# Kernel optimization log

Hardware: AMD Instinct MI355X
Metric: run time of the kernel (lower is better)

## Reference

```python
import jax, jax.numpy as jnp
import numpy as np

C = 512
NUM_HEADS = 8
HEAD_DIM = C // NUM_HEADS  # 64
BN_EPS = 1e-5


def setup_inputs() -> dict:
    key = jax.random.key(0)
    ks = jax.random.split(key, 12)
    B, H, W = 8, 32, 32
    s = 0.02
    return {
        "x": jax.random.normal(ks[0], (B, C, H, W), dtype=jnp.float32),
        "gamma": jnp.ones((C,), jnp.float32),
        "beta": jnp.zeros((C,), jnp.float32),
        "rmean": jnp.zeros((C,), jnp.float32),
        "rvar": jnp.ones((C,), jnp.float32),
        "wq": jax.random.normal(ks[1], (C, C), jnp.float32) * s,
        "bq": jnp.zeros((C,), jnp.float32),
        "wk": jax.random.normal(ks[2], (C, C), jnp.float32) * s,
        "bk": jnp.zeros((C,), jnp.float32),
        "wv": jax.random.normal(ks[3], (C, C), jnp.float32) * s,
        "bv": jnp.zeros((C,), jnp.float32),
        "wp": jax.random.normal(ks[4], (C, C), jnp.float32) * s,
        "bp": jnp.zeros((C,), jnp.float32),
    }


def _conv1x1(w, b, h):
    # 1x1 conv == per-pixel dense: (O,C) x (B,C,H,W) -> (B,O,H,W)
    return jnp.einsum('oc,bchw->bohw', w, h) + b[None, :, None, None]


def reference(x, gamma, beta, rmean, rvar, wq, bq, wk, bk, wv, bv, wp, bp):
    B, Cc, H, W = x.shape
    N = H * W
    # BatchNorm2d (eval mode, running stats)
    inv = gamma / jnp.sqrt(rvar + BN_EPS)
    h = x * inv[None, :, None, None] + (beta - rmean * inv)[None, :, None, None]
    q = _conv1x1(wq, bq, h).reshape(B, NUM_HEADS, HEAD_DIM, N)
    k = _conv1x1(wk, bk, h).reshape(B, NUM_HEADS, HEAD_DIM, N)
    v = _conv1x1(wv, bv, h).reshape(B, NUM_HEADS, HEAD_DIM, N)
    scale = 1.0 / np.sqrt(HEAD_DIM).astype(np.float32)
    attn = jnp.einsum('bhdn,bhdm->bhnm', q, k) * scale  # [B,heads,N,N]
    attn = jnp.clip(attn, -50.0, 50.0)
    attn = jax.nn.softmax(attn, axis=-1)
    out = jnp.einsum('bhnm,bhdm->bhdn', attn, v).reshape(B, Cc, H, W)
    out = _conv1x1(wp, bp, out)
    return x + out
```

## Files before the change

kernel.cpp:

```cpp
#include <hip/hip_runtime.h>
#include <stdint.h>

#define C_DIM 512
#define NHEADS 8
#define HDIM 64
#define BATCH 8
#define NPIX 1024
#define Q_PRESCALE 0.18033688011112042f

typedef __bf16 bf16x8 __attribute__((ext_vector_type(8)));
typedef float f32x4 __attribute__((ext_vector_type(4)));
typedef float f32x16 __attribute__((ext_vector_type(16)));

__device__ __forceinline__ unsigned short f2bf(float f) {
  union { float f; unsigned u; } v; v.f = f;
  unsigned r = v.u + 0x7fffu + ((v.u >> 16) & 1u);
  return (unsigned short)(r >> 16);
}

__device__ __forceinline__ void gl_lds16(const void* g, void* l) {
  __builtin_amdgcn_global_load_lds(
      (__attribute__((address_space(1))) void*)g,
      (__attribute__((address_space(3))) void*)l,
      16, 0, 0);
}

__global__ __launch_bounds__(256) void k_prep(const float* __restrict__ wq,
                                              const float* __restrict__ wk,
                                              const float* __restrict__ wv,
                                              const float* __restrict__ wp,
                                              unsigned short* __restrict__ wbf) {
  const int n = C_DIM * C_DIM;
  for (int i = blockIdx.x * blockDim.x + threadIdx.x; i < 4 * n;
       i += gridDim.x * blockDim.x) {
    const float* src = (i < n) ? wq : (i < 2 * n) ? wk : (i < 3 * n) ? wv : wp;
    wbf[i] = f2bf(src[i & (n - 1)]);
  }
}

__global__ __launch_bounds__(256) void k_bnT(const float* __restrict__ x,
                                             const float* __restrict__ gamma,
                                             const float* __restrict__ beta,
                                             const float* __restrict__ rmean,
                                             const float* __restrict__ rvar,
                                             unsigned short* __restrict__ hbT) {
  __shared__ unsigned short tile[64][72];
  const int b = blockIdx.z, c0 = blockIdx.y * 64, n0 = blockIdx.x * 64;
  const int t = threadIdx.x;
#pragma unroll
  for (int it = 0; it < 4; ++it) {
    int c = it * 16 + (t >> 4);
    int n = (t & 15) * 4;
    const float4 v = *(const float4*)&x[((size_t)b * C_DIM + c0 + c) * NPIX + n0 + n];
    int cc = c0 + c;
    float inv = gamma[cc] * rsqrtf(rvar[cc] + 1e-5f);
    float add = beta[cc] - rmean[cc] * inv;
    tile[c][n + 0] = f2bf(v.x * inv + add);
    tile[c][n + 1] = f2bf(v.y * inv + add);
    tile[c][n + 2] = f2bf(v.z * inv + add);
    tile[c][n + 3] = f2bf(v.w * inv + add);
  }
  __syncthreads();
#pragma unroll
  for (int it = 0; it < 2; ++it) {
    int n = it * 32 + (t >> 3);
    int cj = (t & 7) * 8;
    unsigned short tmp[8];
#pragma unroll
    for (int u = 0; u < 8; ++u) tmp[u] = tile[cj + u][n];
    uint4 pk;
    pk.x = (unsigned)tmp[0] | ((unsigned)tmp[1] << 16);
    pk.y = (unsigned)tmp[2] | ((unsigned)tmp[3] << 16);
    pk.z = (unsigned)tmp[4] | ((unsigned)tmp[5] << 16);
    pk.w = (unsigned)tmp[6] | ((unsigned)tmp[7] << 16);
    *(uint4*)&hbT[((size_t)b * NPIX + n0 + n) * C_DIM + c0 + cj] = pk;
  }
}

__global__ __launch_bounds__(256) void k_qkv(const unsigned short* __restrict__ wbf,
                                             const float* __restrict__ bq,
                                             const float* __restrict__ bk,
                                             const float* __restrict__ bv,
                                             const unsigned short* __restrict__ hbT,
                                             unsigned short* __restrict__ QT,
                                             unsigned short* __restrict__ KT,
                                             unsigned short* __restrict__ Vb) {
  __shared__ unsigned short Atile[128 * 32];
  __shared__ unsigned short Btile[128 * 32];
  const int which = blockIdx.z >> 3;
  const int b = blockIdx.z & 7;
  const int m0 = blockIdx.y * 128, n0 = blockIdx.x * 128;
  const unsigned short* W = wbf + (size_t)which * C_DIM * C_DIM;
  const int t = threadIdx.x, wave = t >> 6, lane = t & 63;
  const int wr = wave >> 1, wc = wave & 1;
  f32x4 acc[4][4] = {};

  const int st_row = lane >> 2;
  const int st_col = (((lane & 3) ^ ((lane >> 3) & 3))) * 8;

  for (int k0 = 0; k0 < C_DIM; k0 += 32) {
    __syncthreads();
#pragma unroll
    for (int it = 0; it < 2; ++it) {
      int q = wave + 4 * it;
      int row = q * 16 + st_row;
      gl_lds16(&W[(size_t)(m0 + row) * C_DIM + k0 + st_col], &Atile[q * 512]);
      gl_lds16(&hbT[((size_t)b * NPIX + n0 + row) * C_DIM + k0 + st_col], &Btile[q * 512]);
    }
    __syncthreads();
    bf16x8 af[4], bfr[4];
#pragma unroll
    for (int i = 0; i < 4; ++i) {
      int row = wr * 64 + i * 16 + (lane & 15);
      af[i] = *(const bf16x8*)&Atile[row * 32 + (((lane >> 4) ^ ((row >> 1) & 3)) * 8)];
    }
#pragma unroll
    for (int j = 0; j < 4; ++j) {
      int row = wc * 64 + j * 16 + (lane & 15);
      bfr[j] = *(const bf16x8*)&Btile[row * 32 + (((lane >> 4) ^ ((row >> 1) & 3)) * 8)];
    }
#pragma unroll
    for (int i = 0; i < 4; ++i)
#pragma unroll
      for (int j = 0; j < 4; ++j)
        acc[i][j] = __builtin_amdgcn_mfma_f32_16x16x32_bf16(af[i], bfr[j], acc[i][j], 0, 0, 0);
  }

  const float* bias = (which == 0) ? bq : (which == 1) ? bk : bv;
  if (which < 2) {
    unsigned short* T = (which == 0) ? QT : KT;
    const float qs = (which == 0) ? Q_PRESCALE : 1.0f;
#pragma unroll
    for (int i = 0; i < 4; ++i) {
      int o = m0 + wr * 64 + i * 16 + (lane >> 4) * 4;
      float b0 = bias[o + 0], b1 = bias[o + 1], b2 = bias[o + 2], b3 = bias[o + 3];
#pragma unroll
      for (int j = 0; j < 4; ++j) {
        int n = n0 + wc * 64 + j * 16 + (lane & 15);
        ushort4 pk;
        pk.x = f2bf((acc[i][j][0] + b0) * qs);
        pk.y = f2bf((acc[i][j][1] + b1) * qs);
        pk.z = f2bf((acc[i][j][2] + b2) * qs);
        pk.w = f2bf((acc[i][j][3] + b3) * qs);
        *(ushort4*)&T[((size_t)b * NPIX + n) * C_DIM + o] = pk;
      }
    }
  } else {
#pragma unroll
    for (int i = 0; i < 4; ++i) {
      int o = m0 + wr * 64 + i * 16 + (lane >> 4) * 4;
#pragma unroll
      for (int j = 0; j < 4; ++j) {
        int n = n0 + wc * 64 + j * 16 + (lane & 15);
#pragma unroll
        for (int r = 0; r < 4; ++r)
          Vb[((size_t)b * C_DIM + o + r) * NPIX + n] = f2bf(acc[i][j][r] + bias[o + r]);
      }
    }
  }
}

__global__ __launch_bounds__(256) void k_attn(const unsigned short* __restrict__ QT,
                                              const unsigned short* __restrict__ KT,
                                              const unsigned short* __restrict__ Vb,
                                              unsigned short* __restrict__ AOT) {
  const int bid = blockIdx.x;
  const int b = bid & 7, h = (bid >> 3) & 7, qt = bid >> 6;
  const int n0 = qt * 128;
  const int lane = threadIdx.x & 63, wave = threadIdx.x >> 6;
  const int l31 = lane & 31, hi = lane >> 5;

  bf16x8 qf[4];
  {
    const unsigned short* qbase =
        QT + ((size_t)b * NPIX + n0 + wave * 32 + l31) * C_DIM + h * HDIM + hi * 8;
#pragma unroll
    for (int kk = 0; kk < 4; ++kk) qf[kk] = *(const bf16x8*)(qbase + kk * 16);
  }

  union { unsigned u[4]; bf16x8 v; } ones;
  ones.u[0] = 0x3F803F80u; ones.u[1] = 0x3F803F80u;
  ones.u[2] = 0x3F803F80u; ones.u[3] = 0x3F803F80u;

  const unsigned short* kbase =
      KT + ((size_t)b * NPIX + l31) * C_DIM + h * HDIM + hi * 8;
  const unsigned short* vbase =
      Vb + ((size_t)b * C_DIM + h * HDIM) * NPIX + hi * 8;

  f32x16 oacc[2] = {};
  f32x16 rsacc = {};

  for (int m0 = 0; m0 < NPIX; m0 += 32) {
    f32x16 s = {};
#pragma unroll
    for (int kk = 0; kk < 4; ++kk) {
      bf16x8 kf = *(const bf16x8*)(kbase + (size_t)m0 * C_DIM + kk * 16);
      s = __builtin_amdgcn_mfma_f32_32x32x16_bf16(kf, qf[kk], s, 0, 0, 0);
    }
    unsigned w[8];
#pragma unroll
    for (int r2 = 0; r2 < 8; ++r2) {
      float e0 = exp2f(s[2 * r2]);
      float e1 = exp2f(s[2 * r2 + 1]);
      asm("v_cvt_pk_bf16_f32 %0, %1, %2" : "=v"(w[r2]) : "v"(e0), "v"(e1));
    }
    asm volatile("v_permlane32_swap_b32 %0, %1" : "+v"(w[0]), "+v"(w[2]));
    asm volatile("v_permlane32_swap_b32 %0, %1" : "+v"(w[1]), "+v"(w[3]));
    asm volatile("v_permlane32_swap_b32 %0, %1" : "+v"(w[4]), "+v"(w[6]));
    asm volatile("v_permlane32_swap_b32 %0, %1" : "+v"(w[5]), "+v"(w[7]));
    union U8 { unsigned u[4]; bf16x8 v; };
    U8 pa0, pa1;
    pa0.u[0] = w[0]; pa0.u[1] = w[1]; pa0.u[2] = w[2]; pa0.u[3] = w[3];
    pa1.u[0] = w[4]; pa1.u[1] = w[5]; pa1.u[2] = w[6]; pa1.u[3] = w[7];
    rsacc = __builtin_amdgcn_mfma_f32_32x32x16_bf16(pa0.v, ones.v, rsacc, 0, 0, 0);
    rsacc = __builtin_amdgcn_mfma_f32_32x32x16_bf16(pa1.v, ones.v, rsacc, 0, 0, 0);
#pragma unroll
    for (int dt = 0; dt < 2; ++dt) {
      const unsigned short* vrow = vbase + (size_t)(dt * 32 + l31) * NPIX + m0;
      bf16x8 v0 = *(const bf16x8*)(vrow);
      bf16x8 v1 = *(const bf16x8*)(vrow + 16);
      oacc[dt] = __builtin_amdgcn_mfma_f32_32x32x16_bf16(pa0.v, v0, oacc[dt], 0, 0, 0);
      oacc[dt] = __builtin_amdgcn_mfma_f32_32x32x16_bf16(pa1.v, v1, oacc[dt], 0, 0, 0);
    }
  }

  float inv[16];
#pragma unroll
  for (int r = 0; r < 16; ++r) inv[r] = 1.0f / rsacc[r];

  __bf16* obase = (__bf16*)(AOT + ((size_t)b * NPIX + n0 + wave * 32) * C_DIM +
                            h * HDIM + l31);
#pragma unroll
  for (int dt = 0; dt < 2; ++dt)
#pragma unroll
    for (int r = 0; r < 16; ++r) {
      int q = (r & 3) + 8 * (r >> 2) + 4 * hi;
      obase[(size_t)q * C_DIM + dt * 32] = (__bf16)(oacc[dt][r] * inv[r]);
    }
}

__global__ __launch_bounds__(256) void k_proj(const unsigned short* __restrict__ Wp,
                                              const float* __restrict__ bp,
                                              const unsigned short* __restrict__ AOT,
                                              const float* __restrict__ x,
                                              float* __restrict__ out) {
  __shared__ unsigned short Atile[128 * 32];
  __shared__ unsigned short Btile[128 * 32];
  const int b = blockIdx.z;
  const int m0 = blockIdx.y * 128, n0 = blockIdx.x * 128;
  const int t = threadIdx.x, wave = t >> 6, lane = t & 63;
  const int wr = wave >> 1, wc = wave & 1;
  f32x4 acc[4][4] = {};
  const int st_row = lane >> 2;
  const int st_col = (((lane & 3) ^ ((lane >> 3) & 3))) * 8;

  for (int k0 = 0; k0 < C_DIM; k0 += 32) {
    __syncthreads();
#pragma unroll
    for (int it = 0; it < 2; ++it) {
      int q = wave + 4 * it;
      int row = q * 16 + st_row;
      gl_lds16(&Wp[(size_t)(m0 + row) * C_DIM + k0 + st_col], &Atile[q * 512]);
      gl_lds16(&AOT[((size_t)b * NPIX + n0 + row) * C_DIM + k0 + st_col], &Btile[q * 512]);
    }
    __syncthreads();
    bf16x8 af[4], bfr[4];
#pragma unroll
    for (int i = 0; i < 4; ++i) {
      int row = wr * 64 + i * 16 + (lane & 15);
      af[i] = *(const bf16x8*)&Atile[row * 32 + (((lane >> 4) ^ ((row >> 1) & 3)) * 8)];
    }
#pragma unroll
    for (int j = 0; j < 4; ++j) {
      int row = wc * 64 + j * 16 + (lane & 15);
      bfr[j] = *(const bf16x8*)&Btile[row * 32 + (((lane >> 4) ^ ((row >> 1) & 3)) * 8)];
    }
#pragma unroll
    for (int i = 0; i < 4; ++i)
#pragma unroll
      for (int j = 0; j < 4; ++j)
        acc[i][j] = __builtin_amdgcn_mfma_f32_16x16x32_bf16(af[i], bfr[j], acc[i][j], 0, 0, 0);
  }

#pragma unroll
  for (int i = 0; i < 4; ++i) {
    int o = m0 + wr * 64 + i * 16 + (lane >> 4) * 4;
    float b0 = bp[o + 0], b1 = bp[o + 1], b2 = bp[o + 2], b3 = bp[o + 3];
#pragma unroll
    for (int j = 0; j < 4; ++j) {
      int n = n0 + wc * 64 + j * 16 + (lane & 15);
      size_t base = ((size_t)b * C_DIM + o) * NPIX + n;
      out[base + 0 * NPIX] = acc[i][j][0] + b0 + x[base + 0 * NPIX];
      out[base + 1 * NPIX] = acc[i][j][1] + b1 + x[base + 1 * NPIX];
      out[base + 2 * NPIX] = acc[i][j][2] + b2 + x[base + 2 * NPIX];
      out[base + 3 * NPIX] = acc[i][j][3] + b3 + x[base + 3 * NPIX];
    }
  }
}

extern "C" void kernel_launch(void* const* d_in, const int* in_sizes, int n_in,
                              void* d_out, int out_size, void* d_ws, size_t ws_size,
                              hipStream_t stream) {
  (void)in_sizes; (void)n_in; (void)out_size; (void)ws_size;
  const float* x     = (const float*)d_in[0];
  const float* gamma = (const float*)d_in[1];
  const float* beta  = (const float*)d_in[2];
  const float* rmean = (const float*)d_in[3];
  const float* rvar  = (const float*)d_in[4];
  const float* wq    = (const float*)d_in[5];
  const float* bq    = (const float*)d_in[6];
  const float* wk    = (const float*)d_in[7];
  const float* bk    = (const float*)d_in[8];
  const float* wv    = (const float*)d_in[9];
  const float* bv    = (const float*)d_in[10];
  const float* wp    = (const float*)d_in[11];
  const float* bp    = (const float*)d_in[12];

  unsigned short* ws  = (unsigned short*)d_ws;
  const size_t WSZ    = (size_t)C_DIM * C_DIM;
  const size_t BIG    = (size_t)BATCH * NPIX * C_DIM;
  unsigned short* wbf = ws;
  unsigned short* hbT = wbf + 4 * WSZ;
  unsigned short* QT  = hbT + BIG;
  unsigned short* KT  = QT + BIG;
  unsigned short* Vb  = KT + BIG;
  unsigned short* AOT = Vb + BIG;

  k_prep<<<dim3(512), dim3(256), 0, stream>>>(wq, wk, wv, wp, wbf);
  k_bnT<<<dim3(16, 8, 8), dim3(256), 0, stream>>>(x, gamma, beta, rmean, rvar, hbT);
  k_qkv<<<dim3(8, 4, 24), dim3(256), 0, stream>>>(wbf, bq, bk, bv, hbT, QT, KT, Vb);
  k_attn<<<dim3(512), dim3(256), 0, stream>>>(QT, KT, Vb, AOT);
  k_proj<<<dim3(8, 4, 8), dim3(256), 0, stream>>>(wbf + 3 * WSZ, bp, AOT, x, (float*)d_out);
}
```

Before: 196.6 us.

## Split attention over key halves with LDS double-buffered K/V and combine pass

```diff
diff --git a/kernel.cpp b/kernel.cpp
--- a/kernel.cpp
+++ b/kernel.cpp
@@ -163,10 +163,16 @@
 __global__ __launch_bounds__(256) void k_attn(const unsigned short* __restrict__ QT,
                                               const unsigned short* __restrict__ KT,
                                               const unsigned short* __restrict__ Vb,
-                                              unsigned short* __restrict__ AOT) {
+                                              unsigned short* __restrict__ OA,
+                                              unsigned short* __restrict__ OB,
+                                              float* __restrict__ rs) {
+  __shared__ unsigned short Ks[2][64 * 64];
+  __shared__ unsigned short Vs[2][64 * 64];
+
   const int bid = blockIdx.x;
-  const int b = bid & 7, h = (bid >> 3) & 7, qt = bid >> 6;
+  const int b = bid & 7, h = (bid >> 3) & 7, qt = (bid >> 6) & 7, ks = bid >> 9;
   const int n0 = qt * 128;
+  const int kbase0 = ks * 512;
   const int lane = threadIdx.x & 63, wave = threadIdx.x >> 6;
   const int l31 = lane & 31, hi = lane >> 5;
 
@@ -182,53 +188,76 @@
   ones.u[0] = 0x3F803F80u; ones.u[1] = 0x3F803F80u;
   ones.u[2] = 0x3F803F80u; ones.u[3] = 0x3F803F80u;
 
-  const unsigned short* kbase =
-      KT + ((size_t)b * NPIX + l31) * C_DIM + h * HDIM + hi * 8;
-  const unsigned short* vbase =
-      Vb + ((size_t)b * C_DIM + h * HDIM) * NPIX + hi * 8;
+  auto stage = [&](int buf, int tile) {
+    const int m0 = kbase0 + tile * 64;
+#pragma unroll
+    for (int it = 0; it < 2; ++it) {
+      int rb = it * 32 + wave * 8;
+      int row = rb + (lane >> 3);
+      int srcc = ((lane & 7) ^ (row & 7)) * 8;
+      gl_lds16(&KT[((size_t)b * NPIX + m0 + row) * C_DIM + h * HDIM + srcc],
+               &Ks[buf][rb * 64]);
+      int srck = ((lane & 7) ^ (row & 7)) * 8;
+      gl_lds16(&Vb[((size_t)b * C_DIM + h * HDIM + row) * NPIX + m0 + srck],
+               &Vs[buf][rb * 64]);
+    }
+  };
 
   f32x16 oacc[2] = {};
   f32x16 rsacc = {};
 
-  for (int m0 = 0; m0 < NPIX; m0 += 32) {
-    f32x16 s = {};
-#pragma unroll
-    for (int kk = 0; kk < 4; ++kk) {
-      bf16x8 kf = *(const bf16x8*)(kbase + (size_t)m0 * C_DIM + kk * 16);
-      s = __builtin_amdgcn_mfma_f32_32x32x16_bf16(kf, qf[kk], s, 0, 0, 0);
-    }
-    unsigned w[8];
-#pragma unroll
-    for (int r2 = 0; r2 < 8; ++r2) {
-      float e0 = exp2f(s[2 * r2]);
-      float e1 = exp2f(s[2 * r2 + 1]);
-      asm("v_cvt_pk_bf16_f32 %0, %1, %2" : "=v"(w[r2]) : "v"(e0), "v"(e1));
-    }
-    asm volatile("v_permlane32_swap_b32 %0, %1" : "+v"(w[0]), "+v"(w[2]));
-    asm volatile("v_permlane32_swap_b32 %0, %1" : "+v"(w[1]), "+v"(w[3]));
-    asm volatile("v_permlane32_swap_b32 %0, %1" : "+v"(w[4]), "+v"(w[6]));
-    asm volatile("v_permlane32_swap_b32 %0, %1" : "+v"(w[5]), "+v"(w[7]));
-    union U8 { unsigned u[4]; bf16x8 v; };
-    U8 pa0, pa1;
-    pa0.u[0] = w[0]; pa0.u[1] = w[1]; pa0.u[2] = w[2]; pa0.u[3] = w[3];
-    pa1.u[0] = w[4]; pa1.u[1] = w[5]; pa1.u[2] = w[6]; pa1.u[3] = w[7];
-    rsacc = __builtin_amdgcn_mfma_f32_32x32x16_bf16(pa0.v, ones.v, rsacc, 0, 0, 0);
-    rsacc = __builtin_amdgcn_mfma_f32_32x32x16_bf16(pa1.v, ones.v, rsacc, 0, 0, 0);
-#pragma unroll
-    for (int dt = 0; dt < 2; ++dt) {
-      const unsigned short* vrow = vbase + (size_t)(dt * 32 + l31) * NPIX + m0;
-      bf16x8 v0 = *(const bf16x8*)(vrow);
-      bf16x8 v1 = *(const bf16x8*)(vrow + 16);
-      oacc[dt] = __builtin_amdgcn_mfma_f32_32x32x16_bf16(pa0.v, v0, oacc[dt], 0, 0, 0);
-      oacc[dt] = __builtin_amdgcn_mfma_f32_32x32x16_bf16(pa1.v, v1, oacc[dt], 0, 0, 0);
-    }
+  stage(0, 0);
+  __syncthreads();
+
+  for (int tile = 0; tile < 8; ++tile) {
+    const int cur = tile & 1;
+    if (tile < 7) stage(cur ^ 1, tile + 1);
+
+#pragma unroll
+    for (int kt = 0; kt < 2; ++kt) {
+      f32x16 s = {};
+#pragma unroll
+      for (int kk = 0; kk < 4; ++kk) {
+        int row = kt * 32 + l31;
+        int phys = (kk * 2 + hi) ^ (row & 7);
+        bf16x8 kf = *(const bf16x8*)&Ks[cur][row * 64 + phys * 8];
+        s = __builtin_amdgcn_mfma_f32_32x32x16_bf16(kf, qf[kk], s, 0, 0, 0);
+      }
+      unsigned w[8];
+#pragma unroll
+      for (int r2 = 0; r2 < 8; ++r2) {
+        float e0 = exp2f(s[2 * r2]);
+        float e1 = exp2f(s[2 * r2 + 1]);
+        asm("v_cvt_pk_bf16_f32 %0, %1, %2" : "=v"(w[r2]) : "v"(e0), "v"(e1));
+      }
+      asm volatile("v_permlane32_swap_b32 %0, %1" : "+v"(w[0]), "+v"(w[2]));
+      asm volatile("v_permlane32_swap_b32 %0, %1" : "+v"(w[1]), "+v"(w[3]));
+      asm volatile("v_permlane32_swap_b32 %0, %1" : "+v"(w[4]), "+v"(w[6]));
+      asm volatile("v_permlane32_swap_b32 %0, %1" : "+v"(w[5]), "+v"(w[7]));
+      union U8 { unsigned u[4]; bf16x8 v; };
+      U8 pa0, pa1;
+      pa0.u[0] = w[0]; pa0.u[1] = w[1]; pa0.u[2] = w[2]; pa0.u[3] = w[3];
+      pa1.u[0] = w[4]; pa1.u[1] = w[5]; pa1.u[2] = w[6]; pa1.u[3] = w[7];
+      rsacc = __builtin_amdgcn_mfma_f32_32x32x16_bf16(pa0.v, ones.v, rsacc, 0, 0, 0);
+      rsacc = __builtin_amdgcn_mfma_f32_32x32x16_bf16(pa1.v, ones.v, rsacc, 0, 0, 0);
+#pragma unroll
+      for (int dt = 0; dt < 2; ++dt) {
+        int d = dt * 32 + l31;
+        bf16x8 v0 = *(const bf16x8*)&Vs[cur][d * 64 + (((kt * 4 + hi) ^ (d & 7)) * 8)];
+        bf16x8 v1 = *(const bf16x8*)&Vs[cur][d * 64 + (((kt * 4 + 2 + hi) ^ (d & 7)) * 8)];
+        oacc[dt] = __builtin_amdgcn_mfma_f32_32x32x16_bf16(pa0.v, v0, oacc[dt], 0, 0, 0);
+        oacc[dt] = __builtin_amdgcn_mfma_f32_32x32x16_bf16(pa1.v, v1, oacc[dt], 0, 0, 0);
+      }
+    }
+    __syncthreads();
   }
 
   float inv[16];
 #pragma unroll
   for (int r = 0; r < 16; ++r) inv[r] = 1.0f / rsacc[r];
 
-  __bf16* obase = (__bf16*)(AOT + ((size_t)b * NPIX + n0 + wave * 32) * C_DIM +
+  unsigned short* obuf = (ks == 0) ? OA : OB;
+  __bf16* obase = (__bf16*)(obuf + ((size_t)b * NPIX + n0 + wave * 32) * C_DIM +
                             h * HDIM + l31);
 #pragma unroll
   for (int dt = 0; dt < 2; ++dt)
@@ -237,6 +266,50 @@
       int q = (r & 3) + 8 * (r >> 2) + 4 * hi;
       obase[(size_t)q * C_DIM + dt * 32] = (__bf16)(oacc[dt][r] * inv[r]);
     }
+  if (l31 == 0) {
+    float* rbase = rs + (((size_t)ks * 8 + b) * 8 + h) * NPIX + n0 + wave * 32;
+#pragma unroll
+    for (int r = 0; r < 16; ++r)
+      rbase[(r & 3) + 8 * (r >> 2) + 4 * hi] = rsacc[r];
+  }
+}
+
+__global__ __launch_bounds__(256) void k_comb(const unsigned short* OA,
+                                              const unsigned short* OB,
+                                              const float* __restrict__ rs,
+                                              unsigned short* AOT) {
+  int i = blockIdx.x * 256 + threadIdx.x;
+  int b = i >> 16;
+  int rem = i & 65535;
+  int n = rem >> 6;
+  int c8 = rem & 63;
+  int h = c8 >> 3;
+  size_t off = ((size_t)b * NPIX + n) * C_DIM + c8 * 8;
+  float rsA = rs[(((size_t)0 * 8 + b) * 8 + h) * NPIX + n];
+  float rsB = rs[(((size_t)1 * 8 + b) * 8 + h) * NPIX + n];
+  float sA = rsA / (rsA + rsB);
+  float sB = 1.0f - sA;
+  uint4 a = *(const uint4*)(OA + off);
+  uint4 bb = *(const uint4*)(OB + off);
+  const unsigned* au = (const unsigned*)&a;
+  const unsigned* bu = (const unsigned*)&bb;
+  uint4 o;
+  unsigned* ou = (unsigned*)&o;
+#pragma unroll
+  for (int j = 0; j < 4; ++j) {
+    float a0, a1, b0, b1;
+    union { unsigned u; float f; } t;
+    t.u = (au[j] & 0xFFFFu) << 16; a0 = t.f;
+    t.u = au[j] & 0xFFFF0000u;     a1 = t.f;
+    t.u = (bu[j] & 0xFFFFu) << 16; b0 = t.f;
+    t.u = bu[j] & 0xFFFF0000u;     b1 = t.f;
+    float o0 = sA * a0 + sB * b0;
+    float o1 = sA * a1 + sB * b1;
+    unsigned pk;
+    asm("v_cvt_pk_bf16_f32 %0, %1, %2" : "=v"(pk) : "v"(o0), "v"(o1));
+    ou[j] = pk;
+  }
+  *(uint4*)(AOT + off) = o;
 }
 
 __global__ __launch_bounds__(256) void k_proj(const unsigned short* __restrict__ Wp,
@@ -325,10 +398,12 @@
   unsigned short* KT  = QT + BIG;
   unsigned short* Vb  = KT + BIG;
   unsigned short* AOT = Vb + BIG;
+  float*          rs  = (float*)(AOT + BIG);
 
   k_prep<<<dim3(512), dim3(256), 0, stream>>>(wq, wk, wv, wp, wbf);
   k_bnT<<<dim3(16, 8, 8), dim3(256), 0, stream>>>(x, gamma, beta, rmean, rvar, hbT);
   k_qkv<<<dim3(8, 4, 24), dim3(256), 0, stream>>>(wbf, bq, bk, bv, hbT, QT, KT, Vb);
-  k_attn<<<dim3(512), dim3(256), 0, stream>>>(QT, KT, Vb, AOT);
+  k_attn<<<dim3(1024), dim3(256), 0, stream>>>(QT, KT, Vb, AOT, hbT, rs);
+  k_comb<<<dim3(2048), dim3(256), 0, stream>>>(AOT, hbT, rs, AOT);
   k_proj<<<dim3(8, 4, 8), dim3(256), 0, stream>>>(wbf + 3 * WSZ, bp, AOT, x, (float*)d_out);
 }
```

After: 176.4 us. 1.11x faster.
